# Performance work log

Hardware: AMD Instinct MI355X
Metric: run time of the kernel (lower is better)

The kernel has to match this reference:

```python
import jax, jax.numpy as jnp
import numpy as np

N_HEADS = 8
D_K = 64
SCALE = D_K ** -0.5


def setup_inputs() -> dict:
    key = jax.random.key(0)
    k1, k2, k3, k4, k5 = jax.random.split(key, 5)
    C = 512
    inner = N_HEADS * D_K  # 512
    return {
        "x": jax.random.normal(k1, (16, C, 32, 32), dtype=jnp.float32),
        "W_qkv": jax.random.normal(k2, (C, 3 * inner), dtype=jnp.float32) * (C ** -0.5),
        "b_qkv": jax.random.normal(k3, (3 * inner,), dtype=jnp.float32) * 0.02,
        "W_out": jax.random.normal(k4, (inner, C), dtype=jnp.float32) * (inner ** -0.5),
        "b_out": jax.random.normal(k5, (C,), dtype=jnp.float32) * 0.02,
    }


def reference(x, W_qkv, b_qkv, W_out, b_out):
    B, C, H, W = x.shape
    N = H * W
    xt = x.reshape(B, C, N).transpose(0, 2, 1)  # (B, N, C) tokens
    qkv = (xt @ W_qkv + b_qkv).reshape(B, N, N_HEADS, 3 * D_K)
    q, k, v = jnp.split(qkv, 3, axis=-1)  # each (B, N, H, d_k)
    # scores over key axis j; softmax along j (original dim=2 of bijh)
    attn = jnp.einsum('bihd,bjhd->bhij', q, k) * SCALE
    attn = jax.nn.softmax(attn, axis=-1)
    res = jnp.einsum('bhij,bjhd->bihd', attn, v).reshape(B, N, N_HEADS * D_K)
    res = res @ W_out + b_out + xt  # out projection + residual (note: GroupNorm unused in source forward)
    return res.transpose(0, 2, 1).reshape(B, C, H, W)
```

## Files before the change

kernel.cpp:

```cpp
#include <hip/hip_runtime.h>
#include <hip/hip_bf16.h>
#include <stdint.h>

#define N_HEADS 8
#define D_K 64
#define SCALE 0.125f

typedef __attribute__((ext_vector_type(4))) float f32x4;
typedef __attribute__((ext_vector_type(16))) float f32x16;
typedef __attribute__((ext_vector_type(8))) short bf16x8;
typedef __attribute__((ext_vector_type(4))) unsigned short u16x4;

#define AS1 __attribute__((address_space(1)))
#define AS3 __attribute__((address_space(3)))

static __device__ __forceinline__ void gload_lds16(const void* g, void* l) {
    __builtin_amdgcn_global_load_lds((const AS1 void*)g, (AS3 void*)l, 16, 0, 0);
}

static __device__ __forceinline__ __hip_bfloat16 f2bf(float f) {
    return __float2bfloat16(f);
}

static __device__ __forceinline__ unsigned short bfbits(float f) {
    return __builtin_bit_cast(unsigned short, __float2bfloat16(f));
}

static __device__ __forceinline__ uint32_t pkbf(float lo, float hi) {
    return (uint32_t)bfbits(lo) | ((uint32_t)bfbits(hi) << 16);
}

__global__ void transpose_bf16(const float* __restrict__ in,
                               __hip_bfloat16* __restrict__ out,
                               int R, int C) {
    __shared__ float tile[32][33];
    const int bz = blockIdx.z;
    const int r0 = blockIdx.y * 32, c0 = blockIdx.x * 32;
    const float* ip = in + (size_t)bz * R * C;
    __hip_bfloat16* op = out + (size_t)bz * R * C;
    const int tx = threadIdx.x, ty = threadIdx.y;
#pragma unroll
    for (int i = 0; i < 4; ++i)
        tile[ty + i * 8][tx] = ip[(size_t)(r0 + ty + i * 8) * C + c0 + tx];
    __syncthreads();
#pragma unroll
    for (int i = 0; i < 4; ++i)
        op[(size_t)(c0 + ty + i * 8) * R + r0 + tx] = f2bf(tile[tx][ty + i * 8]);
}

__device__ __forceinline__ void gemm128_tile(
    const __hip_bfloat16* __restrict__ Abase, int lda,
    const __hip_bfloat16* __restrict__ Bbase, int ldb,
    int K,
    __hip_bfloat16* Atile, __hip_bfloat16* Btile,
    f32x4 (&acc)[4][4]) {
    const int t = threadIdx.x;
    const int w = t >> 6;
    const int l = t & 63;
    const int wr = (w >> 1) * 64, wc = (w & 1) * 64;
    const int fr = l & 15, fq = l >> 4;

#pragma unroll
    for (int m = 0; m < 4; ++m)
#pragma unroll
        for (int n = 0; n < 4; ++n) acc[m][n] = (f32x4)0.f;

    for (int k0 = 0; k0 < K; k0 += 64) {
        __syncthreads();
#pragma unroll
        for (int i = 0; i < 4; ++i) {
            const int tt = t + i * 256;
            const int row = tt >> 3, c16 = tt & 7;
            const char* ga = (const char*)(Abase + (size_t)row * lda + k0) + c16 * 16;
            const char* gb = (const char*)(Bbase + (size_t)row * ldb + k0) + c16 * 16;
            char* la = (char*)Atile + w * 1024 + i * 4096;
            char* lb = (char*)Btile + w * 1024 + i * 4096;
            gload_lds16(ga, la);
            gload_lds16(gb, lb);
        }
        __syncthreads();
#pragma unroll
        for (int kb = 0; kb < 2; ++kb) {
            bf16x8 af[4], bfr[4];
#pragma unroll
            for (int m = 0; m < 4; ++m)
                af[m] = *(const bf16x8*)(Atile + (wr + m * 16 + fr) * 64 + kb * 32 + fq * 8);
#pragma unroll
            for (int n = 0; n < 4; ++n)
                bfr[n] = *(const bf16x8*)(Btile + (wc + n * 16 + fr) * 64 + kb * 32 + fq * 8);
#pragma unroll
            for (int m = 0; m < 4; ++m)
#pragma unroll
                for (int n = 0; n < 4; ++n)
                    acc[m][n] = __builtin_amdgcn_mfma_f32_16x16x32_bf16(af[m], bfr[n], acc[m][n], 0, 0, 0);
        }
    }
}

__global__ __launch_bounds__(256) void qkv_gemm(
    const __hip_bfloat16* __restrict__ xt,
    const __hip_bfloat16* __restrict__ Wqt,
    const float* __restrict__ bias,
    __hip_bfloat16* __restrict__ q_ws,
    __hip_bfloat16* __restrict__ k_ws,
    __hip_bfloat16* __restrict__ v_ws) {
    __shared__ __attribute__((aligned(16))) __hip_bfloat16 Atile[128 * 64];
    __shared__ __attribute__((aligned(16))) __hip_bfloat16 Btile[128 * 64];
    const int tn = blockIdx.x;
    const int tm = blockIdx.y;
    const int b  = blockIdx.z;
    f32x4 acc[4][4];
    gemm128_tile(xt + ((size_t)b * 1024 + tm * 128) * 512, 512,
                 Wqt + (size_t)tn * 128 * 512, 512, 512, Atile, Btile, acc);

    const int t = threadIdx.x, l = t & 63, w = t >> 6;
    const int wr = (w >> 1) * 64, wc = (w & 1) * 64, fr = l & 15, fq = l >> 4;
#pragma unroll
    for (int m = 0; m < 4; ++m) {
#pragma unroll
        for (int n = 0; n < 4; ++n) {
            const int j = tn * 128 + wc + n * 16 + fr;
            const int h = j / 192, rem = j % 192, p = rem / 64, d = rem % 64;
            const float bj = bias[j];
            const size_t bh = (size_t)b * 8 + h;
#pragma unroll
            for (int r = 0; r < 4; ++r) {
                const int nn = tm * 128 + wr + m * 16 + fq * 4 + r;
                const float v = acc[m][n][r] + bj;
                if (p == 0)      q_ws[(bh * 1024 + nn) * 64 + d] = f2bf(v * SCALE);
                else if (p == 1) k_ws[(bh * 1024 + nn) * 64 + d] = f2bf(v);
                else             v_ws[(bh * 64 + d) * 1024 + nn] = f2bf(v);
            }
        }
    }
}

__global__ __launch_bounds__(256) void attn_kernel(
    const __hip_bfloat16* __restrict__ q_ws,
    const __hip_bfloat16* __restrict__ k_ws,
    const __hip_bfloat16* __restrict__ v_ws,
    __hip_bfloat16* __restrict__ ao) {
    __shared__ __attribute__((aligned(16))) __hip_bfloat16 KtS[2][64 * 64];
    __shared__ __attribute__((aligned(16))) __hip_bfloat16 VtS[2][64 * 64];
    __shared__ __attribute__((aligned(16))) __hip_bfloat16 Pq[4][32 * 16];

    const int id = blockIdx.x;
    const int bh = id & 127;
    const int qt = id >> 7;
    const int t = threadIdx.x, l = t & 63, w = t >> 6;
    const int lq = l & 31, hi = l >> 5;
    const int qrow = qt * 128 + w * 32 + lq;
    const int swz = (lq & 7) << 4;

    const __hip_bfloat16* qp = q_ws + ((size_t)bh * 1024 + qrow) * 64;
    bf16x8 qb[4];
#pragma unroll
    for (int s = 0; s < 4; ++s) qb[s] = *(const bf16x8*)(qp + s * 16 + hi * 8);

    f32x16 oacc[2];
    oacc[0] = (f32x16)0.f; oacc[1] = (f32x16)0.f;
    float m = -1e30f, lsum = 0.f;

    const __hip_bfloat16* kbase = k_ws + (size_t)bh * 1024 * 64;
    const __hip_bfloat16* vbase = v_ws + (size_t)bh * 64 * 1024;

    auto stage = [&](int buf, int kt2) {
#pragma unroll
        for (int i = 0; i < 2; ++i) {
            const int tt = t + i * 256;
            const int row = tt >> 3;
            const int sl = (tt & 7) ^ (row & 7);
            char* kd = (char*)&KtS[buf][0] + w * 1024 + i * 4096;
            char* vd = (char*)&VtS[buf][0] + w * 1024 + i * 4096;
            gload_lds16(kbase + (size_t)(kt2 * 64 + row) * 64 + sl * 8, kd);
            gload_lds16(vbase + (size_t)row * 1024 + kt2 * 64 + sl * 8, vd);
        }
    };

    stage(0, 0);
    __syncthreads();

    for (int kt = 0; kt < 16; ++kt) {
        const int cur = kt & 1;
        if (kt < 15) stage(cur ^ 1, kt + 1);

        const char* KtC = (const char*)&KtS[cur][0];
        const char* VtC = (const char*)&VtS[cur][0];

        f32x16 s0 = (f32x16)0.f, s1 = (f32x16)0.f;
        __builtin_amdgcn_s_setprio(1);
#pragma unroll
        for (int s = 0; s < 4; ++s) {
            const int colb = s * 32 + hi * 16;
            bf16x8 k0 = *(const bf16x8*)(KtC + ((lq * 128 + colb) ^ swz));
            bf16x8 k1 = *(const bf16x8*)(KtC + (((32 + lq) * 128 + colb) ^ swz));
            s0 = __builtin_amdgcn_mfma_f32_32x32x16_bf16(k0, qb[s], s0, 0, 0, 0);
            s1 = __builtin_amdgcn_mfma_f32_32x32x16_bf16(k1, qb[s], s1, 0, 0, 0);
        }
        __builtin_amdgcn_s_setprio(0);

        float ma = fmaxf(s0[0], s0[1]), mb = fmaxf(s0[2], s0[3]);
#pragma unroll
        for (int i = 4; i < 16; i += 4) {
            ma = fmaxf(ma, fmaxf(s0[i], s0[i + 1]));
            mb = fmaxf(mb, fmaxf(s0[i + 2], s0[i + 3]));
        }
#pragma unroll
        for (int i = 0; i < 16; i += 4) {
            ma = fmaxf(ma, fmaxf(s1[i], s1[i + 1]));
            mb = fmaxf(mb, fmaxf(s1[i + 2], s1[i + 3]));
        }
        float pmax = fmaxf(ma, mb);
        pmax = fmaxf(pmax, __shfl_xor(pmax, 32, 64));

        if (__any(pmax - m > 8.f)) {
            const float mn = fmaxf(m, pmax);
            const float corr = __expf(m - mn);
            m = mn;
            lsum *= corr;
#pragma unroll
            for (int i = 0; i < 16; ++i) { oacc[0][i] *= corr; oacc[1][i] *= corr; }
        }

        float ls0 = 0.f, ls1 = 0.f;
#pragma unroll
        for (int i = 0; i < 16; ++i) { s0[i] = __expf(s0[i] - m); ls0 += s0[i]; }
#pragma unroll
        for (int i = 0; i < 16; ++i) { s1[i] = __expf(s1[i] - m); ls1 += s1[i]; }
        lsum += ls0 + ls1;

        char* prow = (char*)&Pq[w][0] + lq * 32;
        const int csw = ((lq >> 2) & 1) << 4;
#pragma unroll
        for (int s = 0; s < 4; ++s) {
            const int rb = (s & 1) * 8;
            uint2 W0, W1;
            if (s < 2) {
                W0.x = pkbf(s0[rb + 0], s0[rb + 1]); W0.y = pkbf(s0[rb + 2], s0[rb + 3]);
                W1.x = pkbf(s0[rb + 4], s0[rb + 5]); W1.y = pkbf(s0[rb + 6], s0[rb + 7]);
            } else {
                W0.x = pkbf(s1[rb + 0], s1[rb + 1]); W0.y = pkbf(s1[rb + 2], s1[rb + 3]);
                W1.x = pkbf(s1[rb + 4], s1[rb + 5]); W1.y = pkbf(s1[rb + 6], s1[rb + 7]);
            }
            *(uint2*)(prow + (csw ^ 0) + 8 * hi) = W0;
            *(uint2*)(prow + (csw ^ 16) + 8 * hi) = W1;
            bf16x8 pf = *(const bf16x8*)(prow + (csw ^ (hi << 4)));
            const int colb = s * 32 + hi * 16;
            bf16x8 v0 = *(const bf16x8*)(VtC + ((lq * 128 + colb) ^ swz));
            bf16x8 v1 = *(const bf16x8*)(VtC + (((32 + lq) * 128 + colb) ^ swz));
            __builtin_amdgcn_s_setprio(1);
            oacc[0] = __builtin_amdgcn_mfma_f32_32x32x16_bf16(v0, pf, oacc[0], 0, 0, 0);
            oacc[1] = __builtin_amdgcn_mfma_f32_32x32x16_bf16(v1, pf, oacc[1], 0, 0, 0);
            __builtin_amdgcn_s_setprio(0);
        }

        __syncthreads();
    }

    lsum += __shfl_xor(lsum, 32, 64);
    const float inv = 1.f / lsum;
    const int b = bh >> 3, h = bh & 7;
    __hip_bfloat16* aop = ao + ((size_t)b * 1024 + qrow) * 512 + h * 64;
#pragma unroll
    for (int dd = 0; dd < 2; ++dd)
#pragma unroll
        for (int rg = 0; rg < 4; ++rg) {
            u16x4 pkd;
#pragma unroll
            for (int j = 0; j < 4; ++j)
                pkd[j] = bfbits(oacc[dd][rg * 4 + j] * inv);
            const int d0 = dd * 32 + rg * 8 + hi * 4;
            *(u16x4*)(aop + d0) = pkd;
        }
}

__global__ __launch_bounds__(256) void out_gemm(
    const __hip_bfloat16* __restrict__ Wot,
    const __hip_bfloat16* __restrict__ ao,
    const float* __restrict__ bias,
    const float* __restrict__ x,
    float* __restrict__ out) {
    __shared__ __attribute__((aligned(16))) __hip_bfloat16 Atile[128 * 64];
    __shared__ __attribute__((aligned(16))) __hip_bfloat16 Btile[128 * 64];
    const int tn = blockIdx.x;
    const int tc = blockIdx.y;
    const int b  = blockIdx.z;
    f32x4 acc[4][4];
    gemm128_tile(Wot + (size_t)tc * 128 * 512, 512,
                 ao + ((size_t)b * 1024 + tn * 128) * 512, 512, 512, Atile, Btile, acc);

    const int t = threadIdx.x, l = t & 63, w = t >> 6;
    const int wr = (w >> 1) * 64, wc = (w & 1) * 64, fr = l & 15, fq = l >> 4;
#pragma unroll
    for (int m = 0; m < 4; ++m) {
#pragma unroll
        for (int n = 0; n < 4; ++n) {
            const int nn = tn * 128 + wc + n * 16 + fr;
#pragma unroll
            for (int r = 0; r < 4; ++r) {
                const int c = tc * 128 + wr + m * 16 + fq * 4 + r;
                const size_t idx = ((size_t)b * 512 + c) * 1024 + nn;
                out[idx] = acc[m][n][r] + bias[c] + x[idx];
            }
        }
    }
}

extern "C" void kernel_launch(void* const* d_in, const int* in_sizes, int n_in,
                              void* d_out, int out_size, void* d_ws, size_t ws_size,
                              hipStream_t stream) {
    const float* x     = (const float*)d_in[0];
    const float* W_qkv = (const float*)d_in[1];
    const float* b_qkv = (const float*)d_in[2];
    const float* W_out = (const float*)d_in[3];
    const float* b_out = (const float*)d_in[4];
    float* out = (float*)d_out;

    const int B = 16, C = 512, N = 1024, BH = B * N_HEADS;

    char* ws = (char*)d_ws;
    __hip_bfloat16* xt   = (__hip_bfloat16*)ws; ws += (size_t)B * N * C * 2;
    __hip_bfloat16* Wqt  = (__hip_bfloat16*)ws; ws += (size_t)1536 * 512 * 2;
    __hip_bfloat16* Wot  = (__hip_bfloat16*)ws; ws += (size_t)512 * 512 * 2;
    __hip_bfloat16* q_ws = (__hip_bfloat16*)ws; ws += (size_t)BH * N * 64 * 2;
    __hip_bfloat16* k_ws = (__hip_bfloat16*)ws; ws += (size_t)BH * N * 64 * 2;
    __hip_bfloat16* v_ws = (__hip_bfloat16*)ws; ws += (size_t)BH * 64 * N * 2;
    __hip_bfloat16* ao   = (__hip_bfloat16*)ws; ws += (size_t)B * N * 512 * 2;

    transpose_bf16<<<dim3(N / 32, C / 32, B), dim3(32, 8), 0, stream>>>(x, xt, C, N);
    transpose_bf16<<<dim3(1536 / 32, 512 / 32, 1), dim3(32, 8), 0, stream>>>(W_qkv, Wqt, 512, 1536);
    transpose_bf16<<<dim3(512 / 32, 512 / 32, 1), dim3(32, 8), 0, stream>>>(W_out, Wot, 512, 512);

    qkv_gemm<<<dim3(12, 8, B), 256, 0, stream>>>(xt, Wqt, b_qkv, q_ws, k_ws, v_ws);

    attn_kernel<<<dim3(1024), 256, 0, stream>>>(q_ws, k_ws, v_ws, ao);

    out_gemm<<<dim3(8, 4, B), 256, 0, stream>>>(Wot, ao, b_out, x, out);
}
```

Baseline: 166.2 us.

## Triple-buffer attention K/V loads, fold log2e into Q scale, remap GEMM blocks per XCD

The attention kernel moves from double to triple buffering of K/V tiles. It replaces __syncthreads with explicit vmcnt waits plus barriers, so two tiles of loads stay in flight. The softmax folds log2(e) into the Q scale so it can use exp2f, and it uses 3-input max trees and four partial sums to shorten dependency chains. Both GEMMs switch to a 1D grid with a block-id remap that groups neighbouring tiles onto the same XCD for L2 reuse. This adds LDS use and relies on exact vmcnt counts being correct.

```diff
diff --git a/kernel.cpp b/kernel.cpp
--- a/kernel.cpp
+++ b/kernel.cpp
@@ -4,7 +4,7 @@
 
 #define N_HEADS 8
 #define D_K 64
-#define SCALE 0.125f
+#define QSCALE (0.125f * 1.44269504088896f)
 
 typedef __attribute__((ext_vector_type(4))) float f32x4;
 typedef __attribute__((ext_vector_type(16))) float f32x16;
@@ -28,6 +28,10 @@
 
 static __device__ __forceinline__ uint32_t pkbf(float lo, float hi) {
     return (uint32_t)bfbits(lo) | ((uint32_t)bfbits(hi) << 16);
+}
+
+static __device__ __forceinline__ float fmax3(float a, float b, float c) {
+    return fmaxf(fmaxf(a, b), c);
 }
 
 __global__ void transpose_bf16(const float* __restrict__ in,
@@ -106,9 +110,11 @@
     __hip_bfloat16* __restrict__ v_ws) {
     __shared__ __attribute__((aligned(16))) __hip_bfloat16 Atile[128 * 64];
     __shared__ __attribute__((aligned(16))) __hip_bfloat16 Btile[128 * 64];
-    const int tn = blockIdx.x;
-    const int tm = blockIdx.y;
-    const int b  = blockIdx.z;
+    const int id0 = blockIdx.x;
+    const int wg = (id0 & 7) * 192 + (id0 >> 3);
+    const int tn = wg % 12;
+    const int tm = (wg / 12) & 7;
+    const int b  = wg / 96;
     f32x4 acc[4][4];
     gemm128_tile(xt + ((size_t)b * 1024 + tm * 128) * 512, 512,
                  Wqt + (size_t)tn * 128 * 512, 512, 512, Atile, Btile, acc);
@@ -127,7 +133,7 @@
             for (int r = 0; r < 4; ++r) {
                 const int nn = tm * 128 + wr + m * 16 + fq * 4 + r;
                 const float v = acc[m][n][r] + bj;
-                if (p == 0)      q_ws[(bh * 1024 + nn) * 64 + d] = f2bf(v * SCALE);
+                if (p == 0)      q_ws[(bh * 1024 + nn) * 64 + d] = f2bf(v * QSCALE);
                 else if (p == 1) k_ws[(bh * 1024 + nn) * 64 + d] = f2bf(v);
                 else             v_ws[(bh * 64 + d) * 1024 + nn] = f2bf(v);
             }
@@ -140,8 +146,8 @@
     const __hip_bfloat16* __restrict__ k_ws,
     const __hip_bfloat16* __restrict__ v_ws,
     __hip_bfloat16* __restrict__ ao) {
-    __shared__ __attribute__((aligned(16))) __hip_bfloat16 KtS[2][64 * 64];
-    __shared__ __attribute__((aligned(16))) __hip_bfloat16 VtS[2][64 * 64];
+    __shared__ __attribute__((aligned(16))) __hip_bfloat16 KtS[3][64 * 64];
+    __shared__ __attribute__((aligned(16))) __hip_bfloat16 VtS[3][64 * 64];
     __shared__ __attribute__((aligned(16))) __hip_bfloat16 Pq[4][32 * 16];
 
     const int id = blockIdx.x;
@@ -178,14 +184,16 @@
     };
 
     stage(0, 0);
-    __syncthreads();
+    stage(1, 1);
+    asm volatile("s_waitcnt vmcnt(4)" ::: "memory");
+    __builtin_amdgcn_s_barrier();
+    __builtin_amdgcn_sched_barrier(0);
 
     for (int kt = 0; kt < 16; ++kt) {
-        const int cur = kt & 1;
-        if (kt < 15) stage(cur ^ 1, kt + 1);
-
-        const char* KtC = (const char*)&KtS[cur][0];
-        const char* VtC = (const char*)&VtS[cur][0];
+        if (kt < 14) stage((kt + 2) % 3, kt + 2);
+
+        const char* KtC = (const char*)&KtS[kt % 3][0];
+        const char* VtC = (const char*)&VtS[kt % 3][0];
 
         f32x16 s0 = (f32x16)0.f, s1 = (f32x16)0.f;
         __builtin_amdgcn_s_setprio(1);
@@ -199,35 +207,48 @@
         }
         __builtin_amdgcn_s_setprio(0);
 
-        float ma = fmaxf(s0[0], s0[1]), mb = fmaxf(s0[2], s0[3]);
-#pragma unroll
-        for (int i = 4; i < 16; i += 4) {
-            ma = fmaxf(ma, fmaxf(s0[i], s0[i + 1]));
-            mb = fmaxf(mb, fmaxf(s0[i + 2], s0[i + 3]));
-        }
-#pragma unroll
-        for (int i = 0; i < 16; i += 4) {
-            ma = fmaxf(ma, fmaxf(s1[i], s1[i + 1]));
-            mb = fmaxf(mb, fmaxf(s1[i + 2], s1[i + 3]));
-        }
-        float pmax = fmaxf(ma, mb);
+        float c0 = fmax3(s0[0], s0[1], s0[2]);
+        float c1 = fmax3(s0[4], s0[5], s0[6]);
+        float c2 = fmax3(s0[8], s0[9], s0[10]);
+        float c3 = fmax3(s0[12], s0[13], s0[14]);
+        c0 = fmax3(c0, s0[3], s1[0]);
+        c1 = fmax3(c1, s0[7], s1[4]);
+        c2 = fmax3(c2, s0[11], s1[8]);
+        c3 = fmax3(c3, s0[15], s1[12]);
+        c0 = fmax3(c0, s1[1], s1[2]);
+        c1 = fmax3(c1, s1[5], s1[6]);
+        c2 = fmax3(c2, s1[9], s1[10]);
+        c3 = fmax3(c3, s1[13], s1[14]);
+        c0 = fmax3(c0, s1[3], c1);
+        c2 = fmax3(c2, s1[7], s1[11]);
+        float pmax = fmax3(c0, c2, fmaxf(c3, s1[15]));
         pmax = fmaxf(pmax, __shfl_xor(pmax, 32, 64));
 
         if (__any(pmax - m > 8.f)) {
             const float mn = fmaxf(m, pmax);
-            const float corr = __expf(m - mn);
+            const float corr = exp2f(m - mn);
             m = mn;
             lsum *= corr;
 #pragma unroll
             for (int i = 0; i < 16; ++i) { oacc[0][i] *= corr; oacc[1][i] *= corr; }
         }
 
-        float ls0 = 0.f, ls1 = 0.f;
-#pragma unroll
-        for (int i = 0; i < 16; ++i) { s0[i] = __expf(s0[i] - m); ls0 += s0[i]; }
-#pragma unroll
-        for (int i = 0; i < 16; ++i) { s1[i] = __expf(s1[i] - m); ls1 += s1[i]; }
-        lsum += ls0 + ls1;
+        float la0 = 0.f, la1 = 0.f, la2 = 0.f, la3 = 0.f;
+#pragma unroll
+        for (int i = 0; i < 16; i += 4) {
+            s0[i + 0] = exp2f(s0[i + 0] - m); la0 += s0[i + 0];
+            s0[i + 1] = exp2f(s0[i + 1] - m); la1 += s0[i + 1];
+            s0[i + 2] = exp2f(s0[i + 2] - m); la2 += s0[i + 2];
+            s0[i + 3] = exp2f(s0[i + 3] - m); la3 += s0[i + 3];
+        }
+#pragma unroll
+        for (int i = 0; i < 16; i += 4) {
+            s1[i + 0] = exp2f(s1[i + 0] - m); la0 += s1[i + 0];
+            s1[i + 1] = exp2f(s1[i + 1] - m); la1 += s1[i + 1];
+            s1[i + 2] = exp2f(s1[i + 2] - m); la2 += s1[i + 2];
+            s1[i + 3] = exp2f(s1[i + 3] - m); la3 += s1[i + 3];
+        }
+        lsum += (la0 + la1) + (la2 + la3);
 
         char* prow = (char*)&Pq[w][0] + lq * 32;
         const int csw = ((lq >> 2) & 1) << 4;
@@ -254,7 +275,15 @@
             __builtin_amdgcn_s_setprio(0);
         }
 
-        __syncthreads();
+        if (kt < 14) {
+            asm volatile("s_waitcnt vmcnt(4)" ::: "memory");
+            __builtin_amdgcn_s_barrier();
+            __builtin_amdgcn_sched_barrier(0);
+        } else if (kt == 14) {
+            asm volatile("s_waitcnt vmcnt(0)" ::: "memory");
+            __builtin_amdgcn_s_barrier();
+            __builtin_amdgcn_sched_barrier(0);
+        }
     }
 
     lsum += __shfl_xor(lsum, 32, 64);
@@ -282,9 +311,11 @@
     float* __restrict__ out) {
     __shared__ __attribute__((aligned(16))) __hip_bfloat16 Atile[128 * 64];
     __shared__ __attribute__((aligned(16))) __hip_bfloat16 Btile[128 * 64];
-    const int tn = blockIdx.x;
-    const int tc = blockIdx.y;
-    const int b  = blockIdx.z;
+    const int id0 = blockIdx.x;
+    const int wg = (id0 & 7) * 64 + (id0 >> 3);
+    const int tn = wg & 7;
+    const int tc = (wg >> 3) & 3;
+    const int b  = wg >> 5;
     f32x4 acc[4][4];
     gemm128_tile(Wot + (size_t)tc * 128 * 512, 512,
                  ao + ((size_t)b * 1024 + tn * 128) * 512, 512, 512, Atile, Btile, acc);
@@ -331,9 +362,9 @@
     transpose_bf16<<<dim3(1536 / 32, 512 / 32, 1), dim3(32, 8), 0, stream>>>(W_qkv, Wqt, 512, 1536);
     transpose_bf16<<<dim3(512 / 32, 512 / 32, 1), dim3(32, 8), 0, stream>>>(W_out, Wot, 512, 512);
 
-    qkv_gemm<<<dim3(12, 8, B), 256, 0, stream>>>(xt, Wqt, b_qkv, q_ws, k_ws, v_ws);
+    qkv_gemm<<<dim3(1536), 256, 0, stream>>>(xt, Wqt, b_qkv, q_ws, k_ws, v_ws);
 
     attn_kernel<<<dim3(1024), 256, 0, stream>>>(q_ws, k_ws, v_ws, ao);
 
-    out_gemm<<<dim3(8, 4, B), 256, 0, stream>>>(Wot, ao, b_out, x, out);
-}
+    out_gemm<<<dim3(512), 256, 0, stream>>>(Wot, ao, b_out, x, out);
+}
```

New measurement: 172.8 us. 1.04x slower.
